# Kernel optimization log

Measured on AMD Instinct MI355X. Metric: run time of the kernel, lower is better.

The kernel has to match this reference:

```python
import jax, jax.numpy as jnp
import numpy as np
from jax import lax


def _gru_layer(x, w_ih, w_hh, b_ih, b_hh):
    """PyTorch-style GRU layer (gate order r, z, n). x: [B,T,I] -> ([B,T,H], [B,H])."""
    B, T, _ = x.shape
    H = w_hh.shape[1]
    # Precompute all input-side gate projections in one big GEMM: [B,T,3H]
    xg = jnp.einsum('bti,gi->btg', x, w_ih) + b_ih

    def step(h, xg_t):
        hg = h @ w_hh.T + b_hh                      # [B,3H]
        xr, xz, xn = jnp.split(xg_t, 3, axis=-1)
        hr, hz, hn = jnp.split(hg, 3, axis=-1)
        r = jax.nn.sigmoid(xr + hr)
        z = jax.nn.sigmoid(xz + hz)
        n = jnp.tanh(xn + r * hn)
        h_new = (1.0 - z) * n + z * h
        return h_new, h_new

    h0 = jnp.zeros((B, H), dtype=x.dtype)
    h_last, hs = lax.scan(step, h0, jnp.swapaxes(xg, 0, 1))  # scan over time
    return jnp.swapaxes(hs, 0, 1), h_last


def setup_inputs() -> dict:
    key = jax.random.key(0)
    ks = jax.random.split(key, 13)
    B, T, I, H = 64, 512, 2048, 128

    def u(k, shape, fan_in):
        bound = 1.0 / np.sqrt(fan_in)
        return jax.random.uniform(k, shape, jnp.float32, -bound, bound)

    return {
        'x': jax.random.normal(ks[0], (B, T, I), jnp.float32),
        'w_ih0': u(ks[1], (3 * H, I), H),
        'w_hh0': u(ks[2], (3 * H, H), H),
        'b_ih0': u(ks[3], (3 * H,), H),
        'b_hh0': u(ks[4], (3 * H,), H),
        'w_ih1': u(ks[5], (3 * H, H), H),
        'w_hh1': u(ks[6], (3 * H, H), H),
        'b_ih1': u(ks[7], (3 * H,), H),
        'b_hh1': u(ks[8], (3 * H,), H),
        'w_fc1': u(ks[9], (64, H), H),
        'b_fc1': u(ks[10], (64,), H),
        'w_fc2': u(ks[11], (1, 64), 64),
        'b_fc2': u(ks[12], (1,), 64),
    }


def reference(x, w_ih0, w_hh0, b_ih0, b_hh0, w_ih1, w_hh1, b_ih1, b_hh1,
              w_fc1, b_fc1, w_fc2, b_fc2):
    # 2-layer GRU (inter-layer dropout is identity in eval mode)
    h1_seq, _ = _gru_layer(x, w_ih0, w_hh0, b_ih0, b_hh0)
    _, h_last = _gru_layer(h1_seq, w_ih1, w_hh1, b_ih1, b_hh1)
    # MLP head: fc1 -> ReLU -> (dropout=identity in eval) -> fc2
    y = jax.nn.relu(h_last @ w_fc1.T + b_fc1)
    return y @ w_fc2.T + b_fc2  # [B, 1]
```

## Files before the change

### kernel.cpp

```cpp
#include <hip/hip_runtime.h>
#include <cstdint>
#include <cstddef>

typedef float f32x4 __attribute__((ext_vector_type(4)));
typedef float f32x2 __attribute__((ext_vector_type(2)));
typedef short s16x8 __attribute__((ext_vector_type(8)));
typedef unsigned short u16;

static __device__ __forceinline__ u16 f2bf(float f) {
    uint32_t x = __float_as_uint(f);
    x += 0x7fffu + ((x >> 16) & 1u);
    return (u16)(x >> 16);
}
static __device__ __forceinline__ float bf2f(u16 h) {
    return __uint_as_float(((uint32_t)h) << 16);
}

static __device__ __forceinline__ void bar_lds() {
    asm volatile("s_waitcnt lgkmcnt(0)" ::: "memory");
    __builtin_amdgcn_s_barrier();
    asm volatile("" ::: "memory");
}

__global__ void k_zero(int* __restrict__ p, int n) {
    int i = blockIdx.x * 256 + threadIdx.x;
    if (i < n) p[i] = 0;
}

__global__ void k_split(const float* __restrict__ src, u16* __restrict__ hi,
                        u16* __restrict__ lo, int n) {
    int i = blockIdx.x * 256 + threadIdx.x;
    if (i < n) {
        float f = src[i];
        u16 h = f2bf(f);
        hi[i] = h;
        lo[i] = f2bf(f - bf2f(h));
    }
}

__global__ __launch_bounds__(256, 2)
void k_gemm(const float* __restrict__ A, const u16* __restrict__ Wh,
            const u16* __restrict__ Wl, const float* __restrict__ bias,
            float* __restrict__ C, int K) {
    __shared__ __align__(16) u16 sm[32768];

    const int tid  = threadIdx.x;
    const int lane = tid & 63;
    const int wave = tid >> 6;
    const int wm = wave >> 1, wn = wave & 1;

    int g = blockIdx.x;
    int xcd = g & 7, ix = g >> 3;
    int q3 = ix / 3;
    int mb = xcd + 8 * q3;
    int nb = ix - 3 * q3;
    const long m0 = (long)mb * 128;
    const int  n0 = nb * 128;

    f32x4 acc[4][4];
    const f32x4 vzero = {0.f, 0.f, 0.f, 0.f};
#pragma unroll
    for (int i = 0; i < 4; ++i)
#pragma unroll
        for (int j = 0; j < 4; ++j) acc[i][j] = vzero;

    const int ar = tid >> 1;
    const int ac = (tid & 1) * 16;
    const float* aptr = A + (m0 + ar) * (long)K + ac;
    const int br = tid >> 2;
    const int bc = (tid & 3) * 8;
    const u16* bhp = Wh + (long)(n0 + br) * K + bc;
    const u16* blp = Wl + (long)(n0 + br) * K + bc;

    const int ksteps = K >> 5;
    f32x4 a0, a1, a2, a3;

    {
        a0 = *(const f32x4*)(aptr + 0);
        a1 = *(const f32x4*)(aptr + 4);
        a2 = *(const f32x4*)(aptr + 8);
        a3 = *(const f32x4*)(aptr + 12);
#pragma unroll
        for (int c = 0; c < 2; ++c) {
            const u16* sh = bhp + (long)(c * 64) * K;
            const u16* sl = blp + (long)(c * 64) * K;
            u16* dh = &sm[8192  + c * 2048 + wave * 512];
            u16* dl = &sm[12288 + c * 2048 + wave * 512];
            __builtin_amdgcn_global_load_lds((const __attribute__((address_space(1))) void*)sh,
                                             (__attribute__((address_space(3))) void*)dh, 16, 0, 0);
            __builtin_amdgcn_global_load_lds((const __attribute__((address_space(1))) void*)sl,
                                             (__attribute__((address_space(3))) void*)dl, 16, 0, 0);
        }
        float fr[16] = {a0.x,a0.y,a0.z,a0.w, a1.x,a1.y,a1.z,a1.w,
                        a2.x,a2.y,a2.z,a2.w, a3.x,a3.y,a3.z,a3.w};
        s16x8 h0, h1, l0, l1;
#pragma unroll
        for (int i = 0; i < 8; ++i) {
            u16 hh = f2bf(fr[i]);     h0[i] = (short)hh; l0[i] = (short)f2bf(fr[i] - bf2f(hh));
            u16 hh2 = f2bf(fr[8+i]);  h1[i] = (short)hh2; l1[i] = (short)f2bf(fr[8+i] - bf2f(hh2));
        }
        u16* dh = &sm[ar * 32 + ac];
        u16* dl = &sm[4096 + ar * 32 + ac];
        *(s16x8*)dh = h0; *(s16x8*)(dh + 8) = h1;
        *(s16x8*)dl = l0; *(s16x8*)(dl + 8) = l1;
    }
    __syncthreads();

    for (int ks = 0; ks < ksteps; ++ks) {
        const int cur = ks & 1, nxt = cur ^ 1;
        const bool more = (ks + 1 < ksteps);
        if (more) {
            const int k0 = (ks + 1) << 5;
            a0 = *(const f32x4*)(aptr + k0 + 0);
            a1 = *(const f32x4*)(aptr + k0 + 4);
            a2 = *(const f32x4*)(aptr + k0 + 8);
            a3 = *(const f32x4*)(aptr + k0 + 12);
#pragma unroll
            for (int c = 0; c < 2; ++c) {
                const u16* sh = bhp + (long)(c * 64) * K + k0;
                const u16* sl = blp + (long)(c * 64) * K + k0;
                u16* dh = &sm[nxt * 16384 + 8192  + c * 2048 + wave * 512];
                u16* dl = &sm[nxt * 16384 + 12288 + c * 2048 + wave * 512];
                __builtin_amdgcn_global_load_lds((const __attribute__((address_space(1))) void*)sh,
                                                 (__attribute__((address_space(3))) void*)dh, 16, 0, 0);
                __builtin_amdgcn_global_load_lds((const __attribute__((address_space(1))) void*)sl,
                                                 (__attribute__((address_space(3))) void*)dl, 16, 0, 0);
            }
        }
        {
            const u16* base = &sm[cur * 16384];
            const int koff = (lane >> 4) * 8;
            const int rsel = lane & 15;
            s16x8 ah[4], al[4];
#pragma unroll
            for (int f = 0; f < 4; ++f) {
                int row = wm * 64 + f * 16 + rsel;
                ah[f] = *(const s16x8*)&base[row * 32 + koff];
                al[f] = *(const s16x8*)&base[4096 + row * 32 + koff];
            }
#pragma unroll
            for (int j = 0; j < 4; ++j) {
                int row = wn * 64 + j * 16 + rsel;
                s16x8 bh = *(const s16x8*)&base[8192  + row * 32 + koff];
                s16x8 bl = *(const s16x8*)&base[12288 + row * 32 + koff];
#pragma unroll
                for (int f = 0; f < 4; ++f) {
                    acc[f][j] = __builtin_amdgcn_mfma_f32_16x16x32_bf16(ah[f], bh, acc[f][j], 0, 0, 0);
                    acc[f][j] = __builtin_amdgcn_mfma_f32_16x16x32_bf16(ah[f], bl, acc[f][j], 0, 0, 0);
                    acc[f][j] = __builtin_amdgcn_mfma_f32_16x16x32_bf16(al[f], bh, acc[f][j], 0, 0, 0);
                }
            }
        }
        if (more) {
            float fr[16] = {a0.x,a0.y,a0.z,a0.w, a1.x,a1.y,a1.z,a1.w,
                            a2.x,a2.y,a2.z,a2.w, a3.x,a3.y,a3.z,a3.w};
            s16x8 h0, h1, l0, l1;
#pragma unroll
            for (int i = 0; i < 8; ++i) {
                u16 hh = f2bf(fr[i]);     h0[i] = (short)hh; l0[i] = (short)f2bf(fr[i] - bf2f(hh));
                u16 hh2 = f2bf(fr[8+i]);  h1[i] = (short)hh2; l1[i] = (short)f2bf(fr[8+i] - bf2f(hh2));
            }
            u16* dh = &sm[nxt * 16384 + ar * 32 + ac];
            u16* dl = &sm[nxt * 16384 + 4096 + ar * 32 + ac];
            *(s16x8*)dh = h0; *(s16x8*)(dh + 8) = h1;
            *(s16x8*)dl = l0; *(s16x8*)(dl + 8) = l1;
        }
        __syncthreads();
    }

    const int r0 = (lane >> 4) << 2;
    const int cn = lane & 15;
#pragma unroll
    for (int f = 0; f < 4; ++f) {
        const long mrow = m0 + wm * 64 + f * 16 + r0;
#pragma unroll
        for (int j = 0; j < 4; ++j) {
            const int n = n0 + wn * 64 + j * 16 + cn;
            const float bv = bias[n];
            float* o = C + mrow * 384 + n;
#pragma unroll
            for (int jj = 0; jj < 4; ++jj) o[(long)jj * 384] = acc[f][j][jj] + bv;
        }
    }
}


struct SmemRecur { float hsh[128]; float hp[8][384]; };
struct SmemGemm  { u16 ah[16 * 128]; u16 al[16 * 128]; };
union Smem {
    SmemRecur r;
    SmemGemm  g;
    char force_one_block_per_cu[98304];
};

#define R_ISSUE(BUF, G) do {                                                  \
    const int _G = (G);                                                       \
    if (_G < 128 && tid < 128) {                                              \
        if (!isL0 && (_G & 3) == 0) {                                         \
            if ((tid & 63) == 0) {                                            \
                while (atomicAdd(&waitflag[b * 32 + (_G >> 2)], 0) == 0)      \
                    __builtin_amdgcn_s_sleep(8);                              \
            }                                                                 \
            __threadfence();                                                  \
        }                                                                     \
        const float* _p = xgb + (size_t)(4 * _G) * 384 + tid;                 \
        BUF[0] = _p[0];    BUF[1] = _p[128];   BUF[2]  = _p[256];             \
        BUF[3] = _p[384];  BUF[4] = _p[512];   BUF[5]  = _p[640];             \
        BUF[6] = _p[768];  BUF[7] = _p[896];   BUF[8]  = _p[1024];            \
        BUF[9] = _p[1152]; BUF[10] = _p[1280]; BUF[11] = _p[1408];            \
    } } while (0)

#define R_STEP(T, BUF, J) do {                                                \
    const int _t = (T);                                                       \
    f32x4 _h0 = *(const f32x4*)(sm.hsh + 16 * w + 0);                         \
    f32x4 _h1 = *(const f32x4*)(sm.hsh + 16 * w + 4);                         \
    f32x4 _h2 = *(const f32x4*)(sm.hsh + 16 * w + 8);                         \
    f32x4 _h3 = *(const f32x4*)(sm.hsh + 16 * w + 12);                        \
    float _ha[16];                                                            \
    _ha[0]=_h0[0];  _ha[1]=_h0[1];  _ha[2]=_h0[2];  _ha[3]=_h0[3];            \
    _ha[4]=_h1[0];  _ha[5]=_h1[1];  _ha[6]=_h1[2];  _ha[7]=_h1[3];            \
    _ha[8]=_h2[0];  _ha[9]=_h2[1];  _ha[10]=_h2[2]; _ha[11]=_h2[3];           \
    _ha[12]=_h3[0]; _ha[13]=_h3[1]; _ha[14]=_h3[2]; _ha[15]=_h3[3];           \
    float _s0=0.f,_s1=0.f,_s2=0.f,_s3=0.f,_s4=0.f,_s5=0.f;                    \
    _Pragma("unroll")                                                         \
    for (int _i = 0; _i < 16; ++_i) {                                         \
        const float _hv = _ha[_i];                                            \
        _s0 = fmaf(_hv, wr[0][_i], _s0); _s1 = fmaf(_hv, wr[1][_i], _s1);     \
        _s2 = fmaf(_hv, wr[2][_i], _s2); _s3 = fmaf(_hv, wr[3][_i], _s3);     \
        _s4 = fmaf(_hv, wr[4][_i], _s4); _s5 = fmaf(_hv, wr[5][_i], _s5);     \
    }                                                                         \
    *(f32x2*)&sm.hp[w][g6 + 0] = (f32x2){_s0, _s1};                           \
    *(f32x2*)&sm.hp[w][g6 + 2] = (f32x2){_s2, _s3};                           \
    *(f32x2*)&sm.hp[w][g6 + 4] = (f32x2){_s4, _s5};                           \
    const bool _pub = isL0 && _t > 0 && (_t & 15) == 0;                       \
    if (_pub && tid < 128) asm volatile("s_waitcnt vmcnt(12)" ::: "memory");  \
    bar_lds();                                                                \
    if (_pub && tid == 0) {                                                   \
        __threadfence();                                                      \
        atomicExch(&setflag[b * 32 + ((_t >> 4) - 1)], 1);                    \
    }                                                                         \
    if (tid < 128) {                                                          \
        const int _c = tid;                                                   \
        float _hr = bhr, _hz = bhz, _hn = bhn;                                \
        _Pragma("unroll")                                                     \
        for (int _q = 0; _q < 8; ++_q) {                                      \
            _hr += sm.hp[_q][_c];                                             \
            _hz += sm.hp[_q][128 + _c];                                       \
            _hn += sm.hp[_q][256 + _c];                                       \
        }                                                                     \
        const float _xr = BUF[(J) * 3 + 0];                                   \
        const float _xz = BUF[(J) * 3 + 1];                                   \
        const float _xn = BUF[(J) * 3 + 2];                                   \
        const float _r = 1.f / (1.f + __expf(-(_xr + _hr)));                  \
        const float _z = 1.f / (1.f + __expf(-(_xz + _hz)));                  \
        float _a = _xn + _r * _hn;                                            \
        _a = fminf(fmaxf(_a, -15.f), 15.f);                                   \
        const float _e = __expf(2.f * _a);                                    \
        const float _n = (_e - 1.f) / (_e + 1.f);                             \
        hreg = (1.f - _z) * _n + _z * hreg;                                   \
        sm.hsh[_c] = hreg;                                                    \
        if (isL0) hseq[((size_t)(b * 512 + _t)) * 128 + _c] = hreg;           \
    }                                                                         \
    bar_lds();                                                                \
} while (0)

__device__ __forceinline__ void recur_role(
    bool isL0, int b, const float* __restrict__ xg,
    const float* __restrict__ whh, const float* __restrict__ bhh,
    float* __restrict__ hseq, int* __restrict__ setflag, int* __restrict__ waitflag,
    const float* __restrict__ wfc1, const float* __restrict__ bfc1,
    const float* __restrict__ wfc2, const float* __restrict__ bfc2,
    float* __restrict__ out, SmemRecur& sm)
{
    const int tid  = threadIdx.x;
    const int w    = tid >> 6;
    const int lane = tid & 63;
    const int g6   = 6 * lane;

    float wr[6][16];
#pragma unroll
    for (int j = 0; j < 6; ++j) {
        const float* p = whh + (size_t)(g6 + j) * 128 + 16 * w;
#pragma unroll
        for (int i4 = 0; i4 < 4; ++i4) {
            f32x4 v = *(const f32x4*)(p + 4 * i4);
            wr[j][4*i4+0] = v[0]; wr[j][4*i4+1] = v[1];
            wr[j][4*i4+2] = v[2]; wr[j][4*i4+3] = v[3];
        }
    }
    float bhr = 0.f, bhz = 0.f, bhn = 0.f, hreg = 0.f;
    if (tid < 128) {
        bhr = bhh[tid]; bhz = bhh[128 + tid]; bhn = bhh[256 + tid];
        sm.hsh[tid] = 0.f;
    }
    const float* xgb = xg + (size_t)b * 512 * 384;

    float pA[12], pB[12];
    R_ISSUE(pA, 0);
    R_ISSUE(pB, 1);
    __syncthreads();

    for (int gp = 0; gp < 64; ++gp) {
        const int t0 = gp * 8;
        R_STEP(t0 + 0, pA, 0); R_STEP(t0 + 1, pA, 1);
        R_STEP(t0 + 2, pA, 2); R_STEP(t0 + 3, pA, 3);
        R_ISSUE(pA, 2 * gp + 2);
        R_STEP(t0 + 4, pB, 0); R_STEP(t0 + 5, pB, 1);
        R_STEP(t0 + 6, pB, 2); R_STEP(t0 + 7, pB, 3);
        R_ISSUE(pB, 2 * gp + 3);
    }

    if (isL0) {
        if (tid < 128) asm volatile("s_waitcnt vmcnt(0)" ::: "memory");
        __syncthreads();
        if (tid == 0) { __threadfence(); atomicExch(&setflag[b * 32 + 31], 1); }
    }

    if (!isL0 && tid < 64) {
        const float* wv = wfc1 + tid * 128;
        float acc = bfc1[tid];
#pragma unroll 8
        for (int c = 0; c < 128; ++c) acc = fmaf(sm.hsh[c], wv[c], acc);
        float p = fmaxf(acc, 0.f) * wfc2[tid];
#pragma unroll
        for (int off = 32; off > 0; off >>= 1) p += __shfl_down(p, off);
        if (tid == 0) out[b] = p + bfc2[0];
    }
}

__device__ __forceinline__ void worker_role(
    int wk, const float* __restrict__ h1, float* __restrict__ xg,
    const float* __restrict__ wih1, const float* __restrict__ bih1,
    int* __restrict__ h1flag, int* __restrict__ xgflag, SmemGemm& sm)
{
    const int tid = threadIdx.x, lane = tid & 63, w = tid >> 6;
    const int rsel = lane & 15, koff = (lane >> 4) * 8;

    s16x8 bh[3][4], bl[3][4];
    float bias[3];
#pragma unroll
    for (int nfi = 0; nfi < 3; ++nfi) {
        const int n = (3 * w + nfi) * 16 + rsel;
        bias[nfi] = bih1[n];
#pragma unroll
        for (int ks = 0; ks < 4; ++ks) {
            const float* p = wih1 + n * 128 + ks * 32 + koff;
            f32x4 v0 = *(const f32x4*)p, v1 = *(const f32x4*)(p + 4);
            float fv[8] = {v0[0],v0[1],v0[2],v0[3], v1[0],v1[1],v1[2],v1[3]};
            s16x8 hh, ll;
#pragma unroll
            for (int i = 0; i < 8; ++i) {
                u16 h = f2bf(fv[i]); hh[i] = (short)h; ll[i] = (short)f2bf(fv[i] - bf2f(h));
            }
            bh[nfi][ks] = hh; bl[nfi][ks] = ll;
        }
    }

    for (int j = wk; j < 2048; j += 128) {
        const int c = j >> 6, b = j & 63;
        if (tid == 0) {
            while (atomicAdd(&h1flag[b * 32 + c], 0) == 0) __builtin_amdgcn_s_sleep(8);
            __threadfence();
        }
        __syncthreads();
        if (tid < 256) {
            const int r = tid >> 4, c0 = (tid & 15) * 8;
            const float* p = h1 + ((size_t)(b * 512 + c * 16 + r)) * 128 + c0;
            f32x4 v0 = *(const f32x4*)p, v1 = *(const f32x4*)(p + 4);
            float fv[8] = {v0[0],v0[1],v0[2],v0[3], v1[0],v1[1],v1[2],v1[3]};
            s16x8 hh, ll;
#pragma unroll
            for (int i = 0; i < 8; ++i) {
                u16 h = f2bf(fv[i]); hh[i] = (short)h; ll[i] = (short)f2bf(fv[i] - bf2f(h));
            }
            const int sc = c0 ^ ((r & 7) << 3);
            *(s16x8*)&sm.ah[r * 128 + sc] = hh;
            *(s16x8*)&sm.al[r * 128 + sc] = ll;
        }
        __syncthreads();

        f32x4 acc[3];
        const f32x4 vz = {0.f, 0.f, 0.f, 0.f};
        acc[0] = vz; acc[1] = vz; acc[2] = vz;
#pragma unroll
        for (int ks = 0; ks < 4; ++ks) {
            const int si = rsel * 128 + ((ks * 32 + koff) ^ ((rsel & 7) << 3));
            s16x8 a_h = *(const s16x8*)&sm.ah[si];
            s16x8 a_l = *(const s16x8*)&sm.al[si];
#pragma unroll
            for (int nfi = 0; nfi < 3; ++nfi) {
                acc[nfi] = __builtin_amdgcn_mfma_f32_16x16x32_bf16(a_h, bh[nfi][ks], acc[nfi], 0, 0, 0);
                acc[nfi] = __builtin_amdgcn_mfma_f32_16x16x32_bf16(a_h, bl[nfi][ks], acc[nfi], 0, 0, 0);
                acc[nfi] = __builtin_amdgcn_mfma_f32_16x16x32_bf16(a_l, bh[nfi][ks], acc[nfi], 0, 0, 0);
            }
        }
#pragma unroll
        for (int nfi = 0; nfi < 3; ++nfi) {
            const int n = (3 * w + nfi) * 16 + rsel;
#pragma unroll
            for (int jj = 0; jj < 4; ++jj) {
                const int m = (lane >> 4) * 4 + jj;
                xg[((size_t)(b * 512 + c * 16 + m)) * 384 + n] = acc[nfi][jj] + bias[nfi];
            }
        }
        __syncthreads();
        if (tid == 0) {
            __threadfence();
            atomicExch(&xgflag[b * 32 + c], 1);
        }
    }
}

__global__ __launch_bounds__(512, 2)
void k_fused(float* __restrict__ xg, float* __restrict__ h1,
             const float* __restrict__ whh0, const float* __restrict__ bhh0,
             const float* __restrict__ wih1, const float* __restrict__ bih1,
             const float* __restrict__ whh1, const float* __restrict__ bhh1,
             const float* __restrict__ wfc1, const float* __restrict__ bfc1,
             const float* __restrict__ wfc2, const float* __restrict__ bfc2,
             float* __restrict__ out, int* __restrict__ h1flag, int* __restrict__ xgflag)
{
    __shared__ __align__(16) Smem sm;
    const int bid = blockIdx.x;
    if (bid < 64) {
        recur_role(true, bid, xg, whh0, bhh0, h1, h1flag, nullptr,
                   nullptr, nullptr, nullptr, nullptr, nullptr, sm.r);
    } else if (bid < 128) {
        recur_role(false, bid - 64, xg, whh1, bhh1, nullptr, nullptr, xgflag,
                   wfc1, bfc1, wfc2, bfc2, out, sm.r);
    } else {
        worker_role(bid - 128, h1, xg, wih1, bih1, h1flag, xgflag, sm.g);
    }
}

extern "C" void kernel_launch(void* const* d_in, const int* in_sizes, int n_in,
                              void* d_out, int out_size, void* d_ws, size_t ws_size,
                              hipStream_t stream) {
    const float* x     = (const float*)d_in[0];
    const float* w_ih0 = (const float*)d_in[1];
    const float* w_hh0 = (const float*)d_in[2];
    const float* b_ih0 = (const float*)d_in[3];
    const float* b_hh0 = (const float*)d_in[4];
    const float* w_ih1 = (const float*)d_in[5];
    const float* w_hh1 = (const float*)d_in[6];
    const float* b_ih1 = (const float*)d_in[7];
    const float* b_hh1 = (const float*)d_in[8];
    const float* w_fc1 = (const float*)d_in[9];
    const float* b_fc1 = (const float*)d_in[10];
    const float* w_fc2 = (const float*)d_in[11];
    const float* b_fc2 = (const float*)d_in[12];
    float* out = (float*)d_out;
    (void)in_sizes; (void)n_in; (void)out_size; (void)ws_size;

    char* ws = (char*)d_ws;
    float* xg     = (float*)(ws + 0);
    float* h1     = (float*)(ws + 50331648);
    u16*   w0h    = (u16*)(ws + 67108864);
    u16*   w0l    = (u16*)(ws + 68681728);
    int*   h1flag = (int*)(ws + 70254592);
    int*   xgflag = h1flag + 2048;

    k_zero<<<16, 256, 0, stream>>>(h1flag, 4096);
    k_split<<<3072, 256, 0, stream>>>(w_ih0, w0h, w0l, 384 * 2048);
    k_gemm<<<768, 256, 0, stream>>>(x, w0h, w0l, b_ih0, xg, 2048);
    k_fused<<<256, 512, 0, stream>>>(xg, h1, w_hh0, b_hh0, w_ih1, b_ih1,
                                     w_hh1, b_hh1, w_fc1, b_fc1, w_fc2, b_fc2,
                                     out, h1flag, xgflag);
}
```

Before: 621.9 us.

## Fuse layer-0 input GEMM into persistent kernel with per-timechunk readiness counters

Removes the separate layer-0 input-projection GEMM launch. Its 768 tiles are now computed inside the persistent fused kernel by the layer-1 recurrence blocks (before they start recurring) and by the worker blocks. Layer-0 recurrence blocks wait on a per-time-chunk counter, so the recurrence can start before the whole GEMM finishes. Worker blocks interleave layer-1 input-projection tasks between GEMM k-steps, and W_ih1 is pre-split to bf16 hi/lo by a kernel instead of per block. The risk is that the serial recurrence stalls if GEMM tiles for early time chunks arrive late, and the spin-wait polling adds overhead.

```diff
diff --git a/kernel.cpp b/kernel.cpp
--- a/kernel.cpp
+++ b/kernel.cpp
@@ -15,12 +15,22 @@
 static __device__ __forceinline__ float bf2f(u16 h) {
     return __uint_as_float(((uint32_t)h) << 16);
 }
+static __device__ __forceinline__ void split8(const float* fv, s16x8& hh, s16x8& ll) {
+#pragma unroll
+    for (int i = 0; i < 8; ++i) {
+        u16 h = f2bf(fv[i]); hh[i] = (short)h; ll[i] = (short)f2bf(fv[i] - bf2f(h));
+    }
+}
 
 static __device__ __forceinline__ void bar_lds() {
     asm volatile("s_waitcnt lgkmcnt(0)" ::: "memory");
     __builtin_amdgcn_s_barrier();
     asm volatile("" ::: "memory");
 }
+
+#define GLDS(SRC, DST) __builtin_amdgcn_global_load_lds( \
+    (const __attribute__((address_space(1))) void*)(SRC), \
+    (__attribute__((address_space(3))) void*)(DST), 16, 0, 0)
 
 __global__ void k_zero(int* __restrict__ p, int n) {
     int i = blockIdx.x * 256 + threadIdx.x;
@@ -38,170 +48,210 @@
     }
 }
 
-__global__ __launch_bounds__(256, 2)
-void k_gemm(const float* __restrict__ A, const u16* __restrict__ Wh,
-            const u16* __restrict__ Wl, const float* __restrict__ bias,
-            float* __restrict__ C, int K) {
-    __shared__ __align__(16) u16 sm[32768];
-
-    const int tid  = threadIdx.x;
-    const int lane = tid & 63;
-    const int wave = tid >> 6;
-    const int wm = wave >> 1, wn = wave & 1;
-
-    int g = blockIdx.x;
-    int xcd = g & 7, ix = g >> 3;
-    int q3 = ix / 3;
-    int mb = xcd + 8 * q3;
-    int nb = ix - 3 * q3;
-    const long m0 = (long)mb * 128;
-    const int  n0 = nb * 128;
-
-    f32x4 acc[4][4];
-    const f32x4 vzero = {0.f, 0.f, 0.f, 0.f};
-#pragma unroll
-    for (int i = 0; i < 4; ++i)
-#pragma unroll
-        for (int j = 0; j < 4; ++j) acc[i][j] = vzero;
-
-    const int ar = tid >> 1;
-    const int ac = (tid & 1) * 16;
-    const float* aptr = A + (m0 + ar) * (long)K + ac;
-    const int br = tid >> 2;
-    const int bc = (tid & 3) * 8;
-    const u16* bhp = Wh + (long)(n0 + br) * K + bc;
-    const u16* blp = Wl + (long)(n0 + br) * K + bc;
-
-    const int ksteps = K >> 5;
-    f32x4 a0, a1, a2, a3;
+
+struct SmemRecur { float hsh[128]; float hp[8][384]; };
+struct SmemG0    { u16 buf[2][4][4096]; };
+struct SmemX     { u16 ah[2048]; u16 al[2048]; int decision; };
+struct SmemWorker { SmemG0 g0; SmemX x; };
+union Smem {
+    SmemRecur r;
+    SmemWorker w;
+    char force_one_block_per_cu[98304];
+};
+
+__device__ void do_xg1_task(int j, int* __restrict__ xgflag,
+        const float* __restrict__ h1, float* __restrict__ xg,
+        const u16* __restrict__ w1h, const u16* __restrict__ w1l,
+        const float* __restrict__ bih1, SmemX& smx)
+{
+    const int c = j >> 6, b = j & 63;
+    const int tid = threadIdx.x, lane = tid & 63, wv = tid >> 6;
+    const int rsel = lane & 15, koff = (lane >> 4) * 8;
+
+    if (tid < 256) {
+        const int r = tid >> 4, c0 = (tid & 15) * 8;
+        const float* p = h1 + ((size_t)(b * 512 + c * 16 + r)) * 128 + c0;
+        f32x4 v0 = *(const f32x4*)p, v1 = *(const f32x4*)(p + 4);
+        float fv[8] = {v0[0],v0[1],v0[2],v0[3], v1[0],v1[1],v1[2],v1[3]};
+        s16x8 hh, ll; split8(fv, hh, ll);
+        const int sc = c0 ^ ((r & 7) << 3);
+        *(s16x8*)&smx.ah[r * 128 + sc] = hh;
+        *(s16x8*)&smx.al[r * 128 + sc] = ll;
+    }
+    __syncthreads();
+
+    f32x4 acc[3];
+    const f32x4 vz = {0.f, 0.f, 0.f, 0.f};
+    acc[0] = vz; acc[1] = vz; acc[2] = vz;
+#pragma unroll
+    for (int ks = 0; ks < 4; ++ks) {
+        const int si = rsel * 128 + ((ks * 32 + koff) ^ ((rsel & 7) << 3));
+        s16x8 a_h = *(const s16x8*)&smx.ah[si];
+        s16x8 a_l = *(const s16x8*)&smx.al[si];
+#pragma unroll
+        for (int nf = 0; nf < 3; ++nf) {
+            const int n = (3 * wv + nf) * 16 + rsel;
+            s16x8 bh = *(const s16x8*)&w1h[(size_t)n * 128 + ks * 32 + koff];
+            s16x8 bl = *(const s16x8*)&w1l[(size_t)n * 128 + ks * 32 + koff];
+            acc[nf] = __builtin_amdgcn_mfma_f32_16x16x32_bf16(a_h, bh, acc[nf], 0, 0, 0);
+            acc[nf] = __builtin_amdgcn_mfma_f32_16x16x32_bf16(a_h, bl, acc[nf], 0, 0, 0);
+            acc[nf] = __builtin_amdgcn_mfma_f32_16x16x32_bf16(a_l, bh, acc[nf], 0, 0, 0);
+        }
+    }
+#pragma unroll
+    for (int nf = 0; nf < 3; ++nf) {
+        const int n = (3 * wv + nf) * 16 + rsel;
+        const float bv = bih1[n];
+#pragma unroll
+        for (int jj = 0; jj < 4; ++jj) {
+            const int m = (lane >> 4) * 4 + jj;
+            xg[((size_t)(b * 512 + c * 16 + m)) * 384 + n] = acc[nf][jj] + bv;
+        }
+    }
+    __syncthreads();
+    if (tid == 0) { __threadfence(); atomicExch(&xgflag[b * 32 + c], 1); }
+}
+
+__device__ int drain_ready(int nextq, int cap, int* __restrict__ h1flag,
+        int* __restrict__ xgflag, const float* __restrict__ h1,
+        float* __restrict__ xg, const u16* __restrict__ w1h,
+        const u16* __restrict__ w1l, const float* __restrict__ bih1, SmemX& smx)
+{
+    const int tid = threadIdx.x;
+    for (int it = 0; it < cap && nextq < 2048; ++it) {
+        if (tid == 0) {
+            const int c = nextq >> 6, b = nextq & 63;
+            int v = atomicAdd(&h1flag[b * 32 + c], 0);
+            if (v) __threadfence();
+            smx.decision = v;
+        }
+        __syncthreads();
+        const int go = smx.decision;
+        __syncthreads();
+        if (!go) break;
+        do_xg1_task(nextq, xgflag, h1, xg, w1h, w1l, bih1, smx);
+        nextq += 128;
+    }
+    return nextq;
+}
+
+__device__ __attribute__((noinline)) void g0_tile(int T,
+        const float* __restrict__ x, const u16* __restrict__ w0h,
+        const u16* __restrict__ w0l, const float* __restrict__ bih0,
+        float* __restrict__ xg, int* __restrict__ gemmcnt, SmemG0& g,
+        int* nextq_io, int* h1flag, int* xgflag, const float* h1,
+        const u16* w1h, const u16* w1l, const float* bih1, SmemX* smx)
+{
+    const int tc = T / 24, rem = T - tc * 24;
+    const int bg = rem / 3, nb = rem - bg * 3;
+    const int tid = threadIdx.x, lane = tid & 63, wv = tid >> 6;
+    const int wm = wv >> 2, wn = wv & 3;
+    const int rsel = lane & 15, koff = (lane >> 4) * 8;
+
+    const int ar = tid >> 2, ak = (tid & 3) * 8;
+    const float* aptr = x + ((size_t)(bg * 8 + (ar >> 4)) * 512 + tc * 16 + (ar & 15)) * 2048 + ak;
+    const u16* bhp = w0h + (size_t)(nb * 128 + (tid >> 2)) * 2048 + ak;
+    const u16* blp = w0l + (size_t)(nb * 128 + (tid >> 2)) * 2048 + ak;
+
+    f32x4 acc[4][2];
+    const f32x4 vz = {0.f, 0.f, 0.f, 0.f};
+#pragma unroll
+    for (int f = 0; f < 4; ++f) { acc[f][0] = vz; acc[f][1] = vz; }
 
     {
-        a0 = *(const f32x4*)(aptr + 0);
-        a1 = *(const f32x4*)(aptr + 4);
-        a2 = *(const f32x4*)(aptr + 8);
-        a3 = *(const f32x4*)(aptr + 12);
-#pragma unroll
-        for (int c = 0; c < 2; ++c) {
-            const u16* sh = bhp + (long)(c * 64) * K;
-            const u16* sl = blp + (long)(c * 64) * K;
-            u16* dh = &sm[8192  + c * 2048 + wave * 512];
-            u16* dl = &sm[12288 + c * 2048 + wave * 512];
-            __builtin_amdgcn_global_load_lds((const __attribute__((address_space(1))) void*)sh,
-                                             (__attribute__((address_space(3))) void*)dh, 16, 0, 0);
-            __builtin_amdgcn_global_load_lds((const __attribute__((address_space(1))) void*)sl,
-                                             (__attribute__((address_space(3))) void*)dl, 16, 0, 0);
-        }
-        float fr[16] = {a0.x,a0.y,a0.z,a0.w, a1.x,a1.y,a1.z,a1.w,
-                        a2.x,a2.y,a2.z,a2.w, a3.x,a3.y,a3.z,a3.w};
-        s16x8 h0, h1, l0, l1;
-#pragma unroll
-        for (int i = 0; i < 8; ++i) {
-            u16 hh = f2bf(fr[i]);     h0[i] = (short)hh; l0[i] = (short)f2bf(fr[i] - bf2f(hh));
-            u16 hh2 = f2bf(fr[8+i]);  h1[i] = (short)hh2; l1[i] = (short)f2bf(fr[8+i] - bf2f(hh2));
-        }
-        u16* dh = &sm[ar * 32 + ac];
-        u16* dl = &sm[4096 + ar * 32 + ac];
-        *(s16x8*)dh = h0; *(s16x8*)(dh + 8) = h1;
-        *(s16x8*)dl = l0; *(s16x8*)(dl + 8) = l1;
+        GLDS(bhp, &g.buf[0][2][0] + tid * 8);
+        GLDS(blp, &g.buf[0][3][0] + tid * 8);
+        f32x4 a0 = *(const f32x4*)aptr, a1 = *(const f32x4*)(aptr + 4);
+        float fv[8] = {a0[0],a0[1],a0[2],a0[3], a1[0],a1[1],a1[2],a1[3]};
+        s16x8 hh, ll; split8(fv, hh, ll);
+        *(s16x8*)&g.buf[0][0][ar * 32 + ak] = hh;
+        *(s16x8*)&g.buf[0][1][ar * 32 + ak] = ll;
     }
     __syncthreads();
 
-    for (int ks = 0; ks < ksteps; ++ks) {
+    for (int ks = 0; ks < 64; ++ks) {
         const int cur = ks & 1, nxt = cur ^ 1;
-        const bool more = (ks + 1 < ksteps);
+        const bool more = ks < 63;
+        f32x4 a0, a1;
         if (more) {
-            const int k0 = (ks + 1) << 5;
-            a0 = *(const f32x4*)(aptr + k0 + 0);
+            const int k0 = (ks + 1) * 32;
+            GLDS(bhp + k0, &g.buf[nxt][2][0] + tid * 8);
+            GLDS(blp + k0, &g.buf[nxt][3][0] + tid * 8);
+            a0 = *(const f32x4*)(aptr + k0);
             a1 = *(const f32x4*)(aptr + k0 + 4);
-            a2 = *(const f32x4*)(aptr + k0 + 8);
-            a3 = *(const f32x4*)(aptr + k0 + 12);
-#pragma unroll
-            for (int c = 0; c < 2; ++c) {
-                const u16* sh = bhp + (long)(c * 64) * K + k0;
-                const u16* sl = blp + (long)(c * 64) * K + k0;
-                u16* dh = &sm[nxt * 16384 + 8192  + c * 2048 + wave * 512];
-                u16* dl = &sm[nxt * 16384 + 12288 + c * 2048 + wave * 512];
-                __builtin_amdgcn_global_load_lds((const __attribute__((address_space(1))) void*)sh,
-                                                 (__attribute__((address_space(3))) void*)dh, 16, 0, 0);
-                __builtin_amdgcn_global_load_lds((const __attribute__((address_space(1))) void*)sl,
-                                                 (__attribute__((address_space(3))) void*)dl, 16, 0, 0);
-            }
         }
         {
-            const u16* base = &sm[cur * 16384];
-            const int koff = (lane >> 4) * 8;
-            const int rsel = lane & 15;
-            s16x8 ah[4], al[4];
+            const u16* base = &g.buf[cur][0][0];
+            s16x8 ah[4], al[4], bh2[2], bl2[2];
 #pragma unroll
             for (int f = 0; f < 4; ++f) {
-                int row = wm * 64 + f * 16 + rsel;
+                const int row = wm * 64 + f * 16 + rsel;
                 ah[f] = *(const s16x8*)&base[row * 32 + koff];
                 al[f] = *(const s16x8*)&base[4096 + row * 32 + koff];
             }
 #pragma unroll
-            for (int j = 0; j < 4; ++j) {
-                int row = wn * 64 + j * 16 + rsel;
-                s16x8 bh = *(const s16x8*)&base[8192  + row * 32 + koff];
-                s16x8 bl = *(const s16x8*)&base[12288 + row * 32 + koff];
+            for (int j = 0; j < 2; ++j) {
+                const int row = wn * 32 + j * 16 + rsel;
+                bh2[j] = *(const s16x8*)&base[8192  + row * 32 + koff];
+                bl2[j] = *(const s16x8*)&base[12288 + row * 32 + koff];
+            }
+#pragma unroll
+            for (int j = 0; j < 2; ++j)
 #pragma unroll
                 for (int f = 0; f < 4; ++f) {
-                    acc[f][j] = __builtin_amdgcn_mfma_f32_16x16x32_bf16(ah[f], bh, acc[f][j], 0, 0, 0);
-                    acc[f][j] = __builtin_amdgcn_mfma_f32_16x16x32_bf16(ah[f], bl, acc[f][j], 0, 0, 0);
-                    acc[f][j] = __builtin_amdgcn_mfma_f32_16x16x32_bf16(al[f], bh, acc[f][j], 0, 0, 0);
+                    acc[f][j] = __builtin_amdgcn_mfma_f32_16x16x32_bf16(ah[f], bh2[j], acc[f][j], 0, 0, 0);
+                    acc[f][j] = __builtin_amdgcn_mfma_f32_16x16x32_bf16(ah[f], bl2[j], acc[f][j], 0, 0, 0);
+                    acc[f][j] = __builtin_amdgcn_mfma_f32_16x16x32_bf16(al[f], bh2[j], acc[f][j], 0, 0, 0);
                 }
+        }
+        if (more) {
+            float fv[8] = {a0[0],a0[1],a0[2],a0[3], a1[0],a1[1],a1[2],a1[3]};
+            s16x8 hh, ll; split8(fv, hh, ll);
+            *(s16x8*)&g.buf[nxt][0][ar * 32 + ak] = hh;
+            *(s16x8*)&g.buf[nxt][1][ar * 32 + ak] = ll;
+        }
+        __syncthreads();
+        if (smx != nullptr && (ks == 16 || ks == 32 || ks == 48)) {
+            *nextq_io = drain_ready(*nextq_io, 2, h1flag, xgflag, h1, xg,
+                                    w1h, w1l, bih1, *smx);
+        }
+    }
+
+#pragma unroll
+    for (int f = 0; f < 4; ++f)
+#pragma unroll
+        for (int j = 0; j < 2; ++j) {
+            const int n = nb * 128 + wn * 32 + j * 16 + rsel;
+            const float bv = bih0[n];
+#pragma unroll
+            for (int jj = 0; jj < 4; ++jj) {
+                const int m = wm * 64 + f * 16 + (lane >> 4) * 4 + jj;
+                const size_t row = (size_t)(bg * 8 + (m >> 4)) * 512 + tc * 16 + (m & 15);
+                xg[row * 384 + n] = acc[f][j][jj] + bv;
             }
         }
-        if (more) {
-            float fr[16] = {a0.x,a0.y,a0.z,a0.w, a1.x,a1.y,a1.z,a1.w,
-                            a2.x,a2.y,a2.z,a2.w, a3.x,a3.y,a3.z,a3.w};
-            s16x8 h0, h1, l0, l1;
-#pragma unroll
-            for (int i = 0; i < 8; ++i) {
-                u16 hh = f2bf(fr[i]);     h0[i] = (short)hh; l0[i] = (short)f2bf(fr[i] - bf2f(hh));
-                u16 hh2 = f2bf(fr[8+i]);  h1[i] = (short)hh2; l1[i] = (short)f2bf(fr[8+i] - bf2f(hh2));
-            }
-            u16* dh = &sm[nxt * 16384 + ar * 32 + ac];
-            u16* dl = &sm[nxt * 16384 + 4096 + ar * 32 + ac];
-            *(s16x8*)dh = h0; *(s16x8*)(dh + 8) = h1;
-            *(s16x8*)dl = l0; *(s16x8*)(dl + 8) = l1;
-        }
-        __syncthreads();
-    }
-
-    const int r0 = (lane >> 4) << 2;
-    const int cn = lane & 15;
-#pragma unroll
-    for (int f = 0; f < 4; ++f) {
-        const long mrow = m0 + wm * 64 + f * 16 + r0;
-#pragma unroll
-        for (int j = 0; j < 4; ++j) {
-            const int n = n0 + wn * 64 + j * 16 + cn;
-            const float bv = bias[n];
-            float* o = C + mrow * 384 + n;
-#pragma unroll
-            for (int jj = 0; jj < 4; ++jj) o[(long)jj * 384] = acc[f][j][jj] + bv;
-        }
-    }
-}
-
-
-struct SmemRecur { float hsh[128]; float hp[8][384]; };
-struct SmemGemm  { u16 ah[16 * 128]; u16 al[16 * 128]; };
-union Smem {
-    SmemRecur r;
-    SmemGemm  g;
-    char force_one_block_per_cu[98304];
-};
+    __syncthreads();
+    if (tid == 0) { __threadfence(); atomicAdd(&gemmcnt[tc], 1); }
+}
+
 
 #define R_ISSUE(BUF, G) do {                                                  \
     const int _G = (G);                                                       \
     if (_G < 128 && tid < 128) {                                              \
-        if (!isL0 && (_G & 3) == 0) {                                         \
-            if ((tid & 63) == 0) {                                            \
-                while (atomicAdd(&waitflag[b * 32 + (_G >> 2)], 0) == 0)      \
-                    __builtin_amdgcn_s_sleep(8);                              \
+        if ((_G & 3) == 0) {                                                  \
+            if (isL0) {                                                       \
+                if ((tid & 63) == 0) {                                        \
+                    while (atomicAdd(&gemmcnt[_G >> 2], 0) < 24)              \
+                        __builtin_amdgcn_s_sleep(64);                         \
+                }                                                             \
+                __threadfence();                                              \
+            } else {                                                          \
+                if ((tid & 63) == 0) {                                        \
+                    while (atomicAdd(&waitflag[b * 32 + (_G >> 2)], 0) == 0)  \
+                        __builtin_amdgcn_s_sleep(8);                          \
+                }                                                             \
+                __threadfence();                                              \
             }                                                                 \
-            __threadfence();                                                  \
         }                                                                     \
         const float* _p = xgb + (size_t)(4 * _G) * 384 + tid;                 \
         BUF[0] = _p[0];    BUF[1] = _p[128];   BUF[2]  = _p[256];             \
@@ -264,10 +314,11 @@
     bar_lds();                                                                \
 } while (0)
 
-__device__ __forceinline__ void recur_role(
+__device__ void recur_role(
     bool isL0, int b, const float* __restrict__ xg,
     const float* __restrict__ whh, const float* __restrict__ bhh,
     float* __restrict__ hseq, int* __restrict__ setflag, int* __restrict__ waitflag,
+    int* __restrict__ gemmcnt,
     const float* __restrict__ wfc1, const float* __restrict__ bfc1,
     const float* __restrict__ wfc2, const float* __restrict__ bfc2,
     float* __restrict__ out, SmemRecur& sm)
@@ -276,6 +327,7 @@
     const int w    = tid >> 6;
     const int lane = tid & 63;
     const int g6   = 6 * lane;
+    (void)lane;
 
     float wr[6][16];
 #pragma unroll
@@ -328,108 +380,68 @@
     }
 }
 
-__device__ __forceinline__ void worker_role(
-    int wk, const float* __restrict__ h1, float* __restrict__ xg,
-    const float* __restrict__ wih1, const float* __restrict__ bih1,
-    int* __restrict__ h1flag, int* __restrict__ xgflag, SmemGemm& sm)
-{
-    const int tid = threadIdx.x, lane = tid & 63, w = tid >> 6;
-    const int rsel = lane & 15, koff = (lane >> 4) * 8;
-
-    s16x8 bh[3][4], bl[3][4];
-    float bias[3];
-#pragma unroll
-    for (int nfi = 0; nfi < 3; ++nfi) {
-        const int n = (3 * w + nfi) * 16 + rsel;
-        bias[nfi] = bih1[n];
-#pragma unroll
-        for (int ks = 0; ks < 4; ++ks) {
-            const float* p = wih1 + n * 128 + ks * 32 + koff;
-            f32x4 v0 = *(const f32x4*)p, v1 = *(const f32x4*)(p + 4);
-            float fv[8] = {v0[0],v0[1],v0[2],v0[3], v1[0],v1[1],v1[2],v1[3]};
-            s16x8 hh, ll;
-#pragma unroll
-            for (int i = 0; i < 8; ++i) {
-                u16 h = f2bf(fv[i]); hh[i] = (short)h; ll[i] = (short)f2bf(fv[i] - bf2f(h));
-            }
-            bh[nfi][ks] = hh; bl[nfi][ks] = ll;
-        }
-    }
-
-    for (int j = wk; j < 2048; j += 128) {
-        const int c = j >> 6, b = j & 63;
+__device__ void worker_role(int wk, const float* __restrict__ x,
+        const u16* __restrict__ w0h, const u16* __restrict__ w0l,
+        const float* __restrict__ bih0, float* __restrict__ xg,
+        const float* __restrict__ h1, const u16* __restrict__ w1h,
+        const u16* __restrict__ w1l, const float* __restrict__ bih1,
+        int* __restrict__ gemmcnt, int* __restrict__ h1flag,
+        int* __restrict__ xgflag, SmemWorker& sw)
+{
+    const int tid = threadIdx.x;
+    int nextq = wk;
+
+#pragma unroll 1
+    for (int k = 0; k < 6; ++k) {
+        const int T = 64 + wk + 128 * k;
+        if (T < 768) {
+            g0_tile(T, x, w0h, w0l, bih0, xg, gemmcnt, sw.g0,
+                    &nextq, h1flag, xgflag, h1, w1h, w1l, bih1, &sw.x);
+            nextq = drain_ready(nextq, 4, h1flag, xgflag, h1, xg,
+                                w1h, w1l, bih1, sw.x);
+        }
+    }
+    while (nextq < 2048) {
         if (tid == 0) {
-            while (atomicAdd(&h1flag[b * 32 + c], 0) == 0) __builtin_amdgcn_s_sleep(8);
+            const int c = nextq >> 6, b = nextq & 63;
+            while (atomicAdd(&h1flag[b * 32 + c], 0) == 0)
+                __builtin_amdgcn_s_sleep(8);
             __threadfence();
         }
         __syncthreads();
-        if (tid < 256) {
-            const int r = tid >> 4, c0 = (tid & 15) * 8;
-            const float* p = h1 + ((size_t)(b * 512 + c * 16 + r)) * 128 + c0;
-            f32x4 v0 = *(const f32x4*)p, v1 = *(const f32x4*)(p + 4);
-            float fv[8] = {v0[0],v0[1],v0[2],v0[3], v1[0],v1[1],v1[2],v1[3]};
-            s16x8 hh, ll;
-#pragma unroll
-            for (int i = 0; i < 8; ++i) {
-                u16 h = f2bf(fv[i]); hh[i] = (short)h; ll[i] = (short)f2bf(fv[i] - bf2f(h));
-            }
-            const int sc = c0 ^ ((r & 7) << 3);
-            *(s16x8*)&sm.ah[r * 128 + sc] = hh;
-            *(s16x8*)&sm.al[r * 128 + sc] = ll;
-        }
-        __syncthreads();
-
-        f32x4 acc[3];
-        const f32x4 vz = {0.f, 0.f, 0.f, 0.f};
-        acc[0] = vz; acc[1] = vz; acc[2] = vz;
-#pragma unroll
-        for (int ks = 0; ks < 4; ++ks) {
-            const int si = rsel * 128 + ((ks * 32 + koff) ^ ((rsel & 7) << 3));
-            s16x8 a_h = *(const s16x8*)&sm.ah[si];
-            s16x8 a_l = *(const s16x8*)&sm.al[si];
-#pragma unroll
-            for (int nfi = 0; nfi < 3; ++nfi) {
-                acc[nfi] = __builtin_amdgcn_mfma_f32_16x16x32_bf16(a_h, bh[nfi][ks], acc[nfi], 0, 0, 0);
-                acc[nfi] = __builtin_amdgcn_mfma_f32_16x16x32_bf16(a_h, bl[nfi][ks], acc[nfi], 0, 0, 0);
-                acc[nfi] = __builtin_amdgcn_mfma_f32_16x16x32_bf16(a_l, bh[nfi][ks], acc[nfi], 0, 0, 0);
-            }
-        }
-#pragma unroll
-        for (int nfi = 0; nfi < 3; ++nfi) {
-            const int n = (3 * w + nfi) * 16 + rsel;
-#pragma unroll
-            for (int jj = 0; jj < 4; ++jj) {
-                const int m = (lane >> 4) * 4 + jj;
-                xg[((size_t)(b * 512 + c * 16 + m)) * 384 + n] = acc[nfi][jj] + bias[nfi];
-            }
-        }
-        __syncthreads();
-        if (tid == 0) {
-            __threadfence();
-            atomicExch(&xgflag[b * 32 + c], 1);
-        }
+        do_xg1_task(nextq, xgflag, h1, xg, w1h, w1l, bih1, sw.x);
+        nextq += 128;
     }
 }
 
 __global__ __launch_bounds__(512, 2)
-void k_fused(float* __restrict__ xg, float* __restrict__ h1,
+void k_fused(const float* __restrict__ x, float* __restrict__ xg,
+             float* __restrict__ h1,
+             const u16* __restrict__ w0h, const u16* __restrict__ w0l,
+             const float* __restrict__ bih0,
              const float* __restrict__ whh0, const float* __restrict__ bhh0,
-             const float* __restrict__ wih1, const float* __restrict__ bih1,
+             const u16* __restrict__ w1h, const u16* __restrict__ w1l,
+             const float* __restrict__ bih1,
              const float* __restrict__ whh1, const float* __restrict__ bhh1,
              const float* __restrict__ wfc1, const float* __restrict__ bfc1,
              const float* __restrict__ wfc2, const float* __restrict__ bfc2,
-             float* __restrict__ out, int* __restrict__ h1flag, int* __restrict__ xgflag)
+             float* __restrict__ out, int* __restrict__ gemmcnt,
+             int* __restrict__ h1flag, int* __restrict__ xgflag)
 {
     __shared__ __align__(16) Smem sm;
     const int bid = blockIdx.x;
     if (bid < 64) {
-        recur_role(true, bid, xg, whh0, bhh0, h1, h1flag, nullptr,
+        recur_role(true, bid, xg, whh0, bhh0, h1, h1flag, xgflag, gemmcnt,
                    nullptr, nullptr, nullptr, nullptr, nullptr, sm.r);
     } else if (bid < 128) {
+        g0_tile(bid - 64, x, w0h, w0l, bih0, xg, gemmcnt, sm.w.g0,
+                nullptr, nullptr, nullptr, nullptr, nullptr, nullptr, nullptr,
+                nullptr);
         recur_role(false, bid - 64, xg, whh1, bhh1, nullptr, nullptr, xgflag,
-                   wfc1, bfc1, wfc2, bfc2, out, sm.r);
+                   gemmcnt, wfc1, bfc1, wfc2, bfc2, out, sm.r);
     } else {
-        worker_role(bid - 128, h1, xg, wih1, bih1, h1flag, xgflag, sm.g);
+        worker_role(bid - 128, x, w0h, w0l, bih0, xg, h1, w1h, w1l, bih1,
+                    gemmcnt, h1flag, xgflag, sm.w);
     }
 }
 
@@ -457,13 +469,17 @@
     float* h1     = (float*)(ws + 50331648);
     u16*   w0h    = (u16*)(ws + 67108864);
     u16*   w0l    = (u16*)(ws + 68681728);
-    int*   h1flag = (int*)(ws + 70254592);
+    u16*   w1h    = (u16*)(ws + 70254592);
+    u16*   w1l    = (u16*)(ws + 70352896);
+    int*   h1flag = (int*)(ws + 70451200);
     int*   xgflag = h1flag + 2048;
-
-    k_zero<<<16, 256, 0, stream>>>(h1flag, 4096);
+    int*   gemmcnt = xgflag + 2048;
+
+    k_zero<<<17, 256, 0, stream>>>(h1flag, 4128);
     k_split<<<3072, 256, 0, stream>>>(w_ih0, w0h, w0l, 384 * 2048);
-    k_gemm<<<768, 256, 0, stream>>>(x, w0h, w0l, b_ih0, xg, 2048);
-    k_fused<<<256, 512, 0, stream>>>(xg, h1, w_hh0, b_hh0, w_ih1, b_ih1,
-                                     w_hh1, b_hh1, w_fc1, b_fc1, w_fc2, b_fc2,
-                                     out, h1flag, xgflag);
-}
+    k_split<<<192, 256, 0, stream>>>(w_ih1, w1h, w1l, 384 * 128);
+    k_fused<<<256, 512, 0, stream>>>(x, xg, h1, w0h, w0l, b_ih0, w_hh0, b_hh0,
+                                     w1h, w1l, b_ih1, w_hh1, b_hh1,
+                                     w_fc1, b_fc1, w_fc2, b_fc2,
+                                     out, gemmcnt, h1flag, xgflag);
+}
```

Measured after the change: 1.055 ms. 1.7x slower.

## Restructure GRU recurrence to 4-lane-per-unit dot with shuffle reduction and one barrier

Applied to the files above, without the earlier changes.

Each recurrent step's hidden-state matvec is repartitioned so that four adjacent lanes own one hidden unit across all three gates, holding 96 weights in registers and reducing the partial sums with xor shuffles instead of staging them in LDS. The hidden state is double-buffered in shared memory, which cuts each step from two block barriers to one and removes the cross-wave partial-sum buffer. Input-gate prefetch becomes per-step with a two-step lookahead, and the publish flag for the next layer is set on the last step of each chunk rather than the first step of the following one. The extra register pressure (96 weight registers) and the removal of forceinline on the role functions could affect scheduling and occupancy.

```diff
diff --git a/kernel.cpp b/kernel.cpp
--- a/kernel.cpp
+++ b/kernel.cpp
@@ -3,7 +3,6 @@
 #include <cstddef>
 
 typedef float f32x4 __attribute__((ext_vector_type(4)));
-typedef float f32x2 __attribute__((ext_vector_type(2)));
 typedef short s16x8 __attribute__((ext_vector_type(8)));
 typedef unsigned short u16;
 
@@ -185,86 +184,68 @@
 }
 
 
-struct SmemRecur { float hsh[128]; float hp[8][384]; };
-struct SmemGemm  { u16 ah[16 * 128]; u16 al[16 * 128]; };
+struct SmemRecur { float hsh[2][128]; };
+struct SmemGemm  { u16 ah[2048]; u16 al[2048]; };
 union Smem {
     SmemRecur r;
     SmemGemm  g;
     char force_one_block_per_cu[98304];
 };
 
-#define R_ISSUE(BUF, G) do {                                                  \
-    const int _G = (G);                                                       \
-    if (_G < 128 && tid < 128) {                                              \
-        if (!isL0 && (_G & 3) == 0) {                                         \
+#define R_ISSUE(BUF, T_) do {                                                 \
+    const int _pt = (T_);                                                     \
+    if (_pt < 512) {                                                          \
+        if (!isL0 && (_pt & 15) == 0) {                                       \
             if ((tid & 63) == 0) {                                            \
-                while (atomicAdd(&waitflag[b * 32 + (_G >> 2)], 0) == 0)      \
+                while (atomicAdd(&waitflag[b * 32 + (_pt >> 4)], 0) == 0)     \
                     __builtin_amdgcn_s_sleep(8);                              \
             }                                                                 \
             __threadfence();                                                  \
         }                                                                     \
-        const float* _p = xgb + (size_t)(4 * _G) * 384 + tid;                 \
-        BUF[0] = _p[0];    BUF[1] = _p[128];   BUF[2]  = _p[256];             \
-        BUF[3] = _p[384];  BUF[4] = _p[512];   BUF[5]  = _p[640];             \
-        BUF[6] = _p[768];  BUF[7] = _p[896];   BUF[8]  = _p[1024];            \
-        BUF[9] = _p[1152]; BUF[10] = _p[1280]; BUF[11] = _p[1408];            \
+        const float* _p = xgb + (size_t)_pt * 384 + j;                        \
+        BUF[0] = _p[0]; BUF[1] = _p[128]; BUF[2] = _p[256];                   \
     } } while (0)
 
-#define R_STEP(T, BUF, J) do {                                                \
-    const int _t = (T);                                                       \
-    f32x4 _h0 = *(const f32x4*)(sm.hsh + 16 * w + 0);                         \
-    f32x4 _h1 = *(const f32x4*)(sm.hsh + 16 * w + 4);                         \
-    f32x4 _h2 = *(const f32x4*)(sm.hsh + 16 * w + 8);                         \
-    f32x4 _h3 = *(const f32x4*)(sm.hsh + 16 * w + 12);                        \
-    float _ha[16];                                                            \
-    _ha[0]=_h0[0];  _ha[1]=_h0[1];  _ha[2]=_h0[2];  _ha[3]=_h0[3];            \
-    _ha[4]=_h1[0];  _ha[5]=_h1[1];  _ha[6]=_h1[2];  _ha[7]=_h1[3];            \
-    _ha[8]=_h2[0];  _ha[9]=_h2[1];  _ha[10]=_h2[2]; _ha[11]=_h2[3];           \
-    _ha[12]=_h3[0]; _ha[13]=_h3[1]; _ha[14]=_h3[2]; _ha[15]=_h3[3];           \
-    float _s0=0.f,_s1=0.f,_s2=0.f,_s3=0.f,_s4=0.f,_s5=0.f;                    \
+#define R_STEP(T_, BUF, P_) do {                                              \
+    const int _t = (T_);                                                      \
+    const float* _hb = sm.hsh[P_] + 32 * lq;                                  \
+    float _s0 = 0.f, _s1 = 0.f, _s2 = 0.f;                                    \
     _Pragma("unroll")                                                         \
-    for (int _i = 0; _i < 16; ++_i) {                                         \
-        const float _hv = _ha[_i];                                            \
-        _s0 = fmaf(_hv, wr[0][_i], _s0); _s1 = fmaf(_hv, wr[1][_i], _s1);     \
-        _s2 = fmaf(_hv, wr[2][_i], _s2); _s3 = fmaf(_hv, wr[3][_i], _s3);     \
-        _s4 = fmaf(_hv, wr[4][_i], _s4); _s5 = fmaf(_hv, wr[5][_i], _s5);     \
+    for (int _i = 0; _i < 8; ++_i) {                                          \
+        const f32x4 _hv = *(const f32x4*)(_hb + 4 * ((_i + rot) & 7));        \
+        _Pragma("unroll")                                                     \
+        for (int _e = 0; _e < 4; ++_e) {                                      \
+            _s0 = fmaf(_hv[_e], wr0[_i * 4 + _e], _s0);                       \
+            _s1 = fmaf(_hv[_e], wr1[_i * 4 + _e], _s1);                       \
+            _s2 = fmaf(_hv[_e], wr2[_i * 4 + _e], _s2);                       \
+        }                                                                     \
     }                                                                         \
-    *(f32x2*)&sm.hp[w][g6 + 0] = (f32x2){_s0, _s1};                           \
-    *(f32x2*)&sm.hp[w][g6 + 2] = (f32x2){_s2, _s3};                           \
-    *(f32x2*)&sm.hp[w][g6 + 4] = (f32x2){_s4, _s5};                           \
-    const bool _pub = isL0 && _t > 0 && (_t & 15) == 0;                       \
-    if (_pub && tid < 128) asm volatile("s_waitcnt vmcnt(12)" ::: "memory");  \
+    _s0 += __shfl_xor(_s0, 1); _s1 += __shfl_xor(_s1, 1);                     \
+    _s2 += __shfl_xor(_s2, 1);                                                \
+    _s0 += __shfl_xor(_s0, 2); _s1 += __shfl_xor(_s1, 2);                     \
+    _s2 += __shfl_xor(_s2, 2);                                                \
+    const float _r = 1.f / (1.f + __expf(-(BUF[0] + _s0 + bhr)));             \
+    const float _z = 1.f / (1.f + __expf(-(BUF[1] + _s1 + bhz)));             \
+    float _a = BUF[2] + _r * (_s2 + bhn);                                     \
+    _a = fminf(fmaxf(_a, -15.f), 15.f);                                       \
+    const float _e2 = __expf(2.f * _a);                                       \
+    const float _n = (_e2 - 1.f) / (_e2 + 1.f);                               \
+    hreg = (1.f - _z) * _n + _z * hreg;                                       \
+    if (lq == 0) {                                                            \
+        if (isL0) hseq[((size_t)(b * 512 + _t)) * 128 + j] = hreg;            \
+        sm.hsh[P_ ^ 1][j] = hreg;                                             \
+    }                                                                         \
+    R_ISSUE(BUF, _t + 2);                                                     \
+    const bool _pub = isL0 && ((_t & 15) == 15);                              \
+    if (_pub) asm volatile("s_waitcnt vmcnt(3)" ::: "memory");                \
     bar_lds();                                                                \
     if (_pub && tid == 0) {                                                   \
         __threadfence();                                                      \
-        atomicExch(&setflag[b * 32 + ((_t >> 4) - 1)], 1);                    \
+        atomicExch(&setflag[b * 32 + (_t >> 4)], 1);                          \
     }                                                                         \
-    if (tid < 128) {                                                          \
-        const int _c = tid;                                                   \
-        float _hr = bhr, _hz = bhz, _hn = bhn;                                \
-        _Pragma("unroll")                                                     \
-        for (int _q = 0; _q < 8; ++_q) {                                      \
-            _hr += sm.hp[_q][_c];                                             \
-            _hz += sm.hp[_q][128 + _c];                                       \
-            _hn += sm.hp[_q][256 + _c];                                       \
-        }                                                                     \
-        const float _xr = BUF[(J) * 3 + 0];                                   \
-        const float _xz = BUF[(J) * 3 + 1];                                   \
-        const float _xn = BUF[(J) * 3 + 2];                                   \
-        const float _r = 1.f / (1.f + __expf(-(_xr + _hr)));                  \
-        const float _z = 1.f / (1.f + __expf(-(_xz + _hz)));                  \
-        float _a = _xn + _r * _hn;                                            \
-        _a = fminf(fmaxf(_a, -15.f), 15.f);                                   \
-        const float _e = __expf(2.f * _a);                                    \
-        const float _n = (_e - 1.f) / (_e + 1.f);                             \
-        hreg = (1.f - _z) * _n + _z * hreg;                                   \
-        sm.hsh[_c] = hreg;                                                    \
-        if (isL0) hseq[((size_t)(b * 512 + _t)) * 128 + _c] = hreg;           \
-    }                                                                         \
-    bar_lds();                                                                \
 } while (0)
 
-__device__ __forceinline__ void recur_role(
+__device__ void recur_role(
     bool isL0, int b, const float* __restrict__ xg,
     const float* __restrict__ whh, const float* __restrict__ bhh,
     float* __restrict__ hseq, int* __restrict__ setflag, int* __restrict__ waitflag,
@@ -272,55 +253,50 @@
     const float* __restrict__ wfc2, const float* __restrict__ bfc2,
     float* __restrict__ out, SmemRecur& sm)
 {
-    const int tid  = threadIdx.x;
-    const int w    = tid >> 6;
-    const int lane = tid & 63;
-    const int g6   = 6 * lane;
-
-    float wr[6][16];
-#pragma unroll
-    for (int j = 0; j < 6; ++j) {
-        const float* p = whh + (size_t)(g6 + j) * 128 + 16 * w;
-#pragma unroll
-        for (int i4 = 0; i4 < 4; ++i4) {
-            f32x4 v = *(const f32x4*)(p + 4 * i4);
-            wr[j][4*i4+0] = v[0]; wr[j][4*i4+1] = v[1];
-            wr[j][4*i4+2] = v[2]; wr[j][4*i4+3] = v[3];
-        }
-    }
-    float bhr = 0.f, bhz = 0.f, bhn = 0.f, hreg = 0.f;
-    if (tid < 128) {
-        bhr = bhh[tid]; bhz = bhh[128 + tid]; bhn = bhh[256 + tid];
-        sm.hsh[tid] = 0.f;
-    }
+    const int tid = threadIdx.x;
+    const int j   = tid >> 2;
+    const int lq  = tid & 3;
+    const int rot = 2 * lq;
+
+    float wr0[32], wr1[32], wr2[32];
+    {
+        const float* pr = whh + (size_t)(j)       * 128 + 32 * lq;
+        const float* pz = whh + (size_t)(128 + j) * 128 + 32 * lq;
+        const float* pn = whh + (size_t)(256 + j) * 128 + 32 * lq;
+#pragma unroll
+        for (int i = 0; i < 8; ++i) {
+            const int c4 = 4 * ((i + rot) & 7);
+            f32x4 v0 = *(const f32x4*)(pr + c4);
+            f32x4 v1 = *(const f32x4*)(pz + c4);
+            f32x4 v2 = *(const f32x4*)(pn + c4);
+#pragma unroll
+            for (int e = 0; e < 4; ++e) {
+                wr0[i * 4 + e] = v0[e];
+                wr1[i * 4 + e] = v1[e];
+                wr2[i * 4 + e] = v2[e];
+            }
+        }
+    }
+    const float bhr = bhh[j], bhz = bhh[128 + j], bhn = bhh[256 + j];
+    float hreg = 0.f;
     const float* xgb = xg + (size_t)b * 512 * 384;
 
-    float pA[12], pB[12];
+    if (tid < 128) sm.hsh[0][tid] = 0.f;
+    float pA[3], pB[3];
     R_ISSUE(pA, 0);
     R_ISSUE(pB, 1);
     __syncthreads();
 
-    for (int gp = 0; gp < 64; ++gp) {
-        const int t0 = gp * 8;
-        R_STEP(t0 + 0, pA, 0); R_STEP(t0 + 1, pA, 1);
-        R_STEP(t0 + 2, pA, 2); R_STEP(t0 + 3, pA, 3);
-        R_ISSUE(pA, 2 * gp + 2);
-        R_STEP(t0 + 4, pB, 0); R_STEP(t0 + 5, pB, 1);
-        R_STEP(t0 + 6, pB, 2); R_STEP(t0 + 7, pB, 3);
-        R_ISSUE(pB, 2 * gp + 3);
-    }
-
-    if (isL0) {
-        if (tid < 128) asm volatile("s_waitcnt vmcnt(0)" ::: "memory");
-        __syncthreads();
-        if (tid == 0) { __threadfence(); atomicExch(&setflag[b * 32 + 31], 1); }
+    for (int gp = 0; gp < 256; ++gp) {
+        R_STEP(2 * gp,     pA, 0);
+        R_STEP(2 * gp + 1, pB, 1);
     }
 
     if (!isL0 && tid < 64) {
         const float* wv = wfc1 + tid * 128;
         float acc = bfc1[tid];
 #pragma unroll 8
-        for (int c = 0; c < 128; ++c) acc = fmaf(sm.hsh[c], wv[c], acc);
+        for (int c = 0; c < 128; ++c) acc = fmaf(sm.hsh[0][c], wv[c], acc);
         float p = fmaxf(acc, 0.f) * wfc2[tid];
 #pragma unroll
         for (int off = 32; off > 0; off >>= 1) p += __shfl_down(p, off);
@@ -328,7 +304,7 @@
     }
 }
 
-__device__ __forceinline__ void worker_role(
+__device__ void worker_role(
     int wk, const float* __restrict__ h1, float* __restrict__ xg,
     const float* __restrict__ wih1, const float* __restrict__ bih1,
     int* __restrict__ h1flag, int* __restrict__ xgflag, SmemGemm& sm)
@@ -356,8 +332,8 @@
         }
     }
 
-    for (int j = wk; j < 2048; j += 128) {
-        const int c = j >> 6, b = j & 63;
+    for (int jt = wk; jt < 2048; jt += 128) {
+        const int c = jt >> 6, b = jt & 63;
         if (tid == 0) {
             while (atomicAdd(&h1flag[b * 32 + c], 0) == 0) __builtin_amdgcn_s_sleep(8);
             __threadfence();
```

Measured after the change: 937.0 us. 1.51x slower.
